# Performance work log

Measured on AMD Instinct MI355X. Metric: run time of the kernel, lower is better.

## Reference

```python
import jax, jax.numpy as jnp
import numpy as np

B, T, D, H = 512, 1024, 12, 100


def setup_inputs() -> dict:
    key = jax.random.key(0)
    ks = jax.random.split(key, 5)
    x = jax.random.normal(ks[0], (B, T, D), dtype=jnp.float32)
    Wx = jax.random.normal(ks[1], (D, 4 * H), dtype=jnp.float32) * (1.0 / np.sqrt(D))
    Wh = jax.random.normal(ks[2], (H, 4 * H), dtype=jnp.float32) * (1.0 / np.sqrt(H))
    b = jnp.zeros((4 * H,), dtype=jnp.float32)
    Wd = jax.random.normal(ks[3], (H, D), dtype=jnp.float32) * (1.0 / np.sqrt(H))
    bd = jnp.zeros((D,), dtype=jnp.float32)
    return {"x": x, "Wx": Wx, "Wh": Wh, "b": b, "Wd": Wd, "bd": bd}


def _lstm_seq(x, Wx, Wh, b):
    # Precompute input projection for all timesteps (vectorized GEMM).
    xg = jnp.einsum('btd,dh->bth', x, Wx) + b  # [B, T, 4H]
    xg = jnp.transpose(xg, (1, 0, 2))          # [T, B, 4H] for scan

    def step(carry, xg_t):
        h, c = carry
        z = xg_t + h @ Wh                      # [B, 4H]
        i, f, g, o = jnp.split(z, 4, axis=-1)  # Keras gate order: i, f, c, o
        i = jax.nn.sigmoid(i)
        f = jax.nn.sigmoid(f)
        g = jnp.tanh(g)
        o = jax.nn.sigmoid(o)
        c = f * c + i * g
        h = o * jnp.tanh(c)
        return (h, c), h

    h0 = jnp.zeros((x.shape[0], Wh.shape[0]), dtype=x.dtype)
    c0 = jnp.zeros_like(h0)
    _, hs = jax.lax.scan(step, (h0, c0), xg)   # hs: [T, B, H]
    return jnp.transpose(hs, (1, 0, 2))        # [B, T, H]


def reference(x, Wx, Wh, b, Wd, bd):
    hs = _lstm_seq(x, Wx, Wh, b)               # [B, T, H]
    return jnp.einsum('bth,hd->btd', hs, Wd) + bd  # [B, T, 12]
```

## Files before the change

kernel.cpp:

```cpp
#include <hip/hip_runtime.h>
#include <math.h>

#define T_LEN 1024
#define BATCH 512
#define DIN   12
#define HID   100
#define G4    400
#define MB    4
#define NBLK  (BATCH / MB)
#define AROW  160
#define NW    8
#define NTHR  (NW * 64)
#define CHUNK 64
#define UNROLL 8

typedef _Float16 half8   __attribute__((ext_vector_type(8)));
typedef _Float16 half4_t __attribute__((ext_vector_type(4)));
typedef float    f32x4   __attribute__((ext_vector_type(4)));

static __device__ __forceinline__ float fast_exp2(float v) {
#if __has_builtin(__builtin_amdgcn_exp2f)
    return __builtin_amdgcn_exp2f(v);
#else
    return exp2f(v);
#endif
}
static __device__ __forceinline__ float fast_rcp(float v) {
#if __has_builtin(__builtin_amdgcn_rcpf)
    return __builtin_amdgcn_rcpf(v);
#else
    return 1.0f / v;
#endif
}

__launch_bounds__(NTHR, 2)
__global__ void lstm_mfma_kernel(const float* __restrict__ x,
                                 const float* __restrict__ Wx,
                                 const float* __restrict__ Wh,
                                 const float* __restrict__ b,
                                 const float* __restrict__ Wd,
                                 const float* __restrict__ bd,
                                 float* __restrict__ out) {
    __shared__ __align__(16) char smem[65536];
    const int tid  = threadIdx.x;
    const int wid  = tid >> 6;
    const int lane = tid & 63;
    const int l    = lane & 15;
    const int quad = lane >> 4;
    const int b0   = blockIdx.x * MB;
    const int j    = wid * 16 + l;

    _Float16* stage = (_Float16*)smem;
    half8 bfrag[4][4];
#pragma unroll
    for (int pass = 0; pass < 2; ++pass) {
#pragma unroll
        for (int gg = 0; gg < 2; ++gg) {
            const int G = pass * 2 + gg;
#pragma unroll
            for (int kt = 0; kt < 4; ++kt) {
                half8 v;
#pragma unroll
                for (int jj = 0; jj < 8; ++jj) {
                    const int k = kt * 32 + quad * 8 + jj;
                    float w = 0.f;
                    if (wid < 7) {
                        if (j < HID) {
                            if (k < HID)            w = Wh[k * G4 + G * HID + j];
                            else if (k < HID + DIN) w = Wx[(k - HID) * G4 + G * HID + j];
                        }
                    } else if (G == 0) {
                        if (l < DIN && k < HID)     w = Wd[k * DIN + l];
                    }
                    v[jj] = (_Float16)w;
                }
                *(half8*)&stage[((wid * 8) + (gg * 4 + kt)) * 512 + lane * 8] = v;
            }
        }
        __syncthreads();
#pragma unroll
        for (int gg = 0; gg < 2; ++gg)
#pragma unroll
            for (int kt = 0; kt < 4; ++kt)
                bfrag[pass * 2 + gg][kt] =
                    *(half8*)&stage[((wid * 8) + (gg * 4 + kt)) * 512 + lane * 8];
        __syncthreads();
    }

    f32x4 biasC[4];
#pragma unroll
    for (int G = 0; G < 4; ++G) biasC[G] = (f32x4){0.f, 0.f, 0.f, 0.f};
    if (wid < 7) {
        if (j < HID) {
#pragma unroll
            for (int G = 0; G < 4; ++G) {
                const float bv = b[G * HID + j];
                biasC[G] = (f32x4){bv, bv, bv, bv};
            }
        }
    } else if (l < DIN) {
        const float bv = bd[l];
        biasC[0] = (f32x4){bv, bv, bv, bv};
    }

    _Float16 (*Ah)[MB][AROW] = (_Float16 (*)[MB][AROW])smem;
    _Float16* xchunk = (_Float16*)(smem + 2560);

    auto refill = [&](int c) {
#pragma unroll
        for (int ii = 0; ii < 2; ++ii) {
            const int f = tid + NTHR * ii;
            if (f < (CHUNK * MB * DIN) / 4) {
                const int m  = f / (CHUNK * DIN / 4);
                const int o  = f - m * (CHUNK * DIN / 4);
                const int tt = o / 3;
                const int dd = o - tt * 3;
                const float4 v = *(const float4*)(x +
                    ((size_t)(b0 + m) * T_LEN + c * CHUNK + tt) * DIN + dd * 4);
                half4_t h4;
                h4[0] = (_Float16)v.x; h4[1] = (_Float16)v.y;
                h4[2] = (_Float16)v.z; h4[3] = (_Float16)v.w;
                *(half4_t*)&xchunk[tt * (MB * DIN) + m * DIN + dd * 4] = h4;
            }
        }
    };

    for (int i = tid; i < (2 * MB * AROW) / 2; i += NTHR) ((int*)smem)[i] = 0;
    refill(0);
    __syncthreads();
    if (tid < MB * 3) {
        const int m = tid / 3, part = tid - (tid / 3) * 3;
        *(half4_t*)&Ah[0][m][HID + part * 4] =
            *(const half4_t*)&xchunk[m * DIN + part * 4];
    }
    __syncthreads();

    const bool gate_lane = (wid < 7) && (j < HID);
    const int  arow = l >> 2;
    const float L2E = 1.4426950408889634f;

    float c = 0.f;
    float obuf[UNROLL];

#pragma unroll 1
    for (int tb = 0; tb < T_LEN / UNROLL; ++tb) {
#pragma unroll
        for (int it = 0; it < UNROLL; ++it) {
            const int t  = tb * UNROLL + it;
            const int p  = it & 1;
            const int pn = p ^ 1;

            if (it == UNROLL - 1) {
                if (((tb + 1) & 7) == 0 && (tb + 1) < T_LEN / UNROLL) {
                    refill((tb + 1) >> 3);
                    __syncthreads();
                }
            }

            half8 a[4];
#pragma unroll
            for (int kt = 0; kt < 4; ++kt)
                a[kt] = *(const half8*)&Ah[p][arow][kt * 32 + quad * 8];

            if (wid < 7) {
                f32x4 acc[4];
#pragma unroll
                for (int kt = 0; kt < 4; ++kt)
#pragma unroll
                    for (int G = 0; G < 4; ++G)
                        acc[G] = __builtin_amdgcn_mfma_f32_16x16x32_f16(
                                     a[kt], bfrag[G][kt],
                                     (kt == 0) ? biasC[G] : acc[G], 0, 0, 0);

                if (gate_lane) {
                    const float ei = fast_exp2(-L2E * acc[0][0]);
                    const float ef = fast_exp2(-L2E * acc[1][0]);
                    const float eg = fast_exp2(-2.f * L2E * acc[2][0]);
                    const float eo = fast_exp2(-L2E * acc[3][0]);
                    const float gig = (1.f - eg) * fast_rcp((1.f + ei) * (1.f + eg));
                    const float gf  = fast_rcp(1.f + ef);
                    const float cn  = gf * c + gig;
                    c = cn;
                    const float ec = fast_exp2(-2.f * L2E * cn);
                    const float hv = (1.f - ec) * fast_rcp((1.f + eo) * (1.f + ec));
                    Ah[pn][quad][j] = (_Float16)hv;
                }
            } else {
                f32x4 accP;
#pragma unroll
                for (int kt = 0; kt < 4; ++kt)
                    accP = __builtin_amdgcn_mfma_f32_16x16x32_f16(
                               a[kt], bfrag[0][kt],
                               (kt == 0) ? biasC[0] : accP, 0, 0, 0);
                obuf[it] = accP[0];
                if ((t + 1) < T_LEN && lane < MB * 3) {
                    const int m = lane / 3, part = lane - (lane / 3) * 3;
                    *(half4_t*)&Ah[pn][m][HID + part * 4] =
                        *(const half4_t*)&xchunk[((t + 1) & (CHUNK - 1)) * (MB * DIN)
                                                 + m * DIN + part * 4];
                }
            }
            __syncthreads();
        }
        if (wid == 7 && l < DIN) {
#pragma unroll
            for (int s = 0; s < UNROLL; ++s) {
                const int row = tb * UNROLL + s - 1;
                if (row >= 0)
                    out[((size_t)(b0 + quad) * T_LEN + row) * DIN + l] = obuf[s];
            }
        }
    }

    if (wid == 7) {
        half8 a[4];
#pragma unroll
        for (int kt = 0; kt < 4; ++kt)
            a[kt] = *(const half8*)&Ah[0][arow][kt * 32 + quad * 8];
        f32x4 accP;
#pragma unroll
        for (int kt = 0; kt < 4; ++kt)
            accP = __builtin_amdgcn_mfma_f32_16x16x32_f16(
                       a[kt], bfrag[0][kt],
                       (kt == 0) ? biasC[0] : accP, 0, 0, 0);
        if (l < DIN)
            out[((size_t)(b0 + quad) * T_LEN + (T_LEN - 1)) * DIN + l] = accP[0];
    }
}

extern "C" void kernel_launch(void* const* d_in, const int* in_sizes, int n_in,
                              void* d_out, int out_size, void* d_ws, size_t ws_size,
                              hipStream_t stream) {
    const float* x  = (const float*)d_in[0];
    const float* Wx = (const float*)d_in[1];
    const float* Wh = (const float*)d_in[2];
    const float* b  = (const float*)d_in[3];
    const float* Wd = (const float*)d_in[4];
    const float* bd = (const float*)d_in[5];
    float* out = (float*)d_out;

    lstm_mfma_kernel<<<NBLK, NTHR, 0, stream>>>(x, Wx, Wh, b, Wd, bd, out);
}
```

Baseline: 536.4 us.

## Break MFMA accumulation chains, prescale gate weights, use lighter LDS barriers

Folds the -log2(e) (and -2log2(e) for the g gate) scaling into the weights and biases so the gate exponents need no multiply. The cell state is kept in the scaled domain. Each k-tile MFMA now writes an independent accumulator and the partial sums are added in scalar code, which removes the dependent MFMA chain on the serial recurrence path. __syncthreads is replaced by an lgkmcnt-only wait plus s_barrier. Output stores are also issued per step rather than buffered, trading more register pressure and a few extra adds for lower per-timestep latency.

```diff
diff --git a/kernel.cpp b/kernel.cpp
--- a/kernel.cpp
+++ b/kernel.cpp
@@ -31,6 +31,13 @@
 #else
     return 1.0f / v;
 #endif
+}
+
+static __device__ __forceinline__ void wg_barrier_lds() {
+    __builtin_amdgcn_sched_barrier(0);
+    asm volatile("s_waitcnt lgkmcnt(0)" ::: "memory");
+    __builtin_amdgcn_s_barrier();
+    __builtin_amdgcn_sched_barrier(0);
 }
 
 __launch_bounds__(NTHR, 2)
@@ -50,6 +57,8 @@
     const int b0   = blockIdx.x * MB;
     const int j    = wid * 16 + l;
 
+    const float L2E = 1.4426950408889634f;
+
     _Float16* stage = (_Float16*)smem;
     half8 bfrag[4][4];
 #pragma unroll
@@ -57,6 +66,7 @@
 #pragma unroll
         for (int gg = 0; gg < 2; ++gg) {
             const int G = pass * 2 + gg;
+            const float gsc = (G == 2) ? (-2.f * L2E) : (-L2E);
 #pragma unroll
             for (int kt = 0; kt < 4; ++kt) {
                 half8 v;
@@ -66,8 +76,8 @@
                     float w = 0.f;
                     if (wid < 7) {
                         if (j < HID) {
-                            if (k < HID)            w = Wh[k * G4 + G * HID + j];
-                            else if (k < HID + DIN) w = Wx[(k - HID) * G4 + G * HID + j];
+                            if (k < HID)            w = Wh[k * G4 + G * HID + j] * gsc;
+                            else if (k < HID + DIN) w = Wx[(k - HID) * G4 + G * HID + j] * gsc;
                         }
                     } else if (G == 0) {
                         if (l < DIN && k < HID)     w = Wd[k * DIN + l];
@@ -94,7 +104,8 @@
         if (j < HID) {
 #pragma unroll
             for (int G = 0; G < 4; ++G) {
-                const float bv = b[G * HID + j];
+                const float gsc = (G == 2) ? (-2.f * L2E) : (-L2E);
+                const float bv = b[G * HID + j] * gsc;
                 biasC[G] = (f32x4){bv, bv, bv, bv};
             }
         }
@@ -137,10 +148,9 @@
 
     const bool gate_lane = (wid < 7) && (j < HID);
     const int  arow = l >> 2;
-    const float L2E = 1.4426950408889634f;
-
-    float c = 0.f;
-    float obuf[UNROLL];
+    const f32x4 kZ = (f32x4){0.f, 0.f, 0.f, 0.f};
+
+    float cs = 0.f;
 
 #pragma unroll 1
     for (int tb = 0; tb < T_LEN / UNROLL; ++tb) {
@@ -153,7 +163,7 @@
             if (it == UNROLL - 1) {
                 if (((tb + 1) & 7) == 0 && (tb + 1) < T_LEN / UNROLL) {
                     refill((tb + 1) >> 3);
-                    __syncthreads();
+                    wg_barrier_lds();
                 }
             }
 
@@ -163,36 +173,41 @@
                 a[kt] = *(const half8*)&Ah[p][arow][kt * 32 + quad * 8];
 
             if (wid < 7) {
-                f32x4 acc[4];
+                f32x4 dg[4][4];
 #pragma unroll
                 for (int kt = 0; kt < 4; ++kt)
 #pragma unroll
                     for (int G = 0; G < 4; ++G)
-                        acc[G] = __builtin_amdgcn_mfma_f32_16x16x32_f16(
-                                     a[kt], bfrag[G][kt],
-                                     (kt == 0) ? biasC[G] : acc[G], 0, 0, 0);
+                        dg[G][kt] = __builtin_amdgcn_mfma_f32_16x16x32_f16(
+                                        a[kt], bfrag[G][kt],
+                                        (kt == 0) ? biasC[G] : kZ, 0, 0, 0);
 
                 if (gate_lane) {
-                    const float ei = fast_exp2(-L2E * acc[0][0]);
-                    const float ef = fast_exp2(-L2E * acc[1][0]);
-                    const float eg = fast_exp2(-2.f * L2E * acc[2][0]);
-                    const float eo = fast_exp2(-L2E * acc[3][0]);
-                    const float gig = (1.f - eg) * fast_rcp((1.f + ei) * (1.f + eg));
+                    const float zi = (dg[0][0][0] + dg[0][1][0]) + (dg[0][2][0] + dg[0][3][0]);
+                    const float zf = (dg[1][0][0] + dg[1][1][0]) + (dg[1][2][0] + dg[1][3][0]);
+                    const float zg = (dg[2][0][0] + dg[2][1][0]) + (dg[2][2][0] + dg[2][3][0]);
+                    const float zo = (dg[3][0][0] + dg[3][1][0]) + (dg[3][2][0] + dg[3][3][0]);
+                    const float ei = fast_exp2(zi);
+                    const float ef = fast_exp2(zf);
+                    const float eg = fast_exp2(zg);
+                    const float eo = fast_exp2(zo);
                     const float gf  = fast_rcp(1.f + ef);
-                    const float cn  = gf * c + gig;
-                    c = cn;
-                    const float ec = fast_exp2(-2.f * L2E * cn);
+                    const float dd  = (1.f + ei) * (1.f + eg);
+                    const float u   = __builtin_fmaf(eg, 2.f * L2E, -2.f * L2E);
+                    const float gig = u * fast_rcp(dd);
+                    cs = __builtin_fmaf(gf, cs, gig);
+                    const float ec = fast_exp2(cs);
                     const float hv = (1.f - ec) * fast_rcp((1.f + eo) * (1.f + ec));
                     Ah[pn][quad][j] = (_Float16)hv;
                 }
             } else {
-                f32x4 accP;
-#pragma unroll
-                for (int kt = 0; kt < 4; ++kt)
-                    accP = __builtin_amdgcn_mfma_f32_16x16x32_f16(
-                               a[kt], bfrag[0][kt],
-                               (kt == 0) ? biasC[0] : accP, 0, 0, 0);
-                obuf[it] = accP[0];
+                f32x4 p0 = __builtin_amdgcn_mfma_f32_16x16x32_f16(a[0], bfrag[0][0], biasC[0], 0, 0, 0);
+                f32x4 p1 = __builtin_amdgcn_mfma_f32_16x16x32_f16(a[1], bfrag[0][1], kZ, 0, 0, 0);
+                f32x4 p2 = __builtin_amdgcn_mfma_f32_16x16x32_f16(a[2], bfrag[0][2], kZ, 0, 0, 0);
+                f32x4 p3 = __builtin_amdgcn_mfma_f32_16x16x32_f16(a[3], bfrag[0][3], kZ, 0, 0, 0);
+                const float ov = (p0[0] + p1[0]) + (p2[0] + p3[0]);
+                if (t >= 1 && l < DIN)
+                    out[((size_t)(b0 + quad) * T_LEN + (t - 1)) * DIN + l] = ov;
                 if ((t + 1) < T_LEN && lane < MB * 3) {
                     const int m = lane / 3, part = lane - (lane / 3) * 3;
                     *(half4_t*)&Ah[pn][m][HID + part * 4] =
@@ -200,15 +215,7 @@
                                                  + m * DIN + part * 4];
                 }
             }
-            __syncthreads();
-        }
-        if (wid == 7 && l < DIN) {
-#pragma unroll
-            for (int s = 0; s < UNROLL; ++s) {
-                const int row = tb * UNROLL + s - 1;
-                if (row >= 0)
-                    out[((size_t)(b0 + quad) * T_LEN + row) * DIN + l] = obuf[s];
-            }
+            wg_barrier_lds();
         }
     }
 
@@ -217,14 +224,13 @@
 #pragma unroll
         for (int kt = 0; kt < 4; ++kt)
             a[kt] = *(const half8*)&Ah[0][arow][kt * 32 + quad * 8];
-        f32x4 accP;
-#pragma unroll
-        for (int kt = 0; kt < 4; ++kt)
-            accP = __builtin_amdgcn_mfma_f32_16x16x32_f16(
-                       a[kt], bfrag[0][kt],
-                       (kt == 0) ? biasC[0] : accP, 0, 0, 0);
+        f32x4 p0 = __builtin_amdgcn_mfma_f32_16x16x32_f16(a[0], bfrag[0][0], biasC[0], 0, 0, 0);
+        f32x4 p1 = __builtin_amdgcn_mfma_f32_16x16x32_f16(a[1], bfrag[0][1], kZ, 0, 0, 0);
+        f32x4 p2 = __builtin_amdgcn_mfma_f32_16x16x32_f16(a[2], bfrag[0][2], kZ, 0, 0, 0);
+        f32x4 p3 = __builtin_amdgcn_mfma_f32_16x16x32_f16(a[3], bfrag[0][3], kZ, 0, 0, 0);
+        const float ov = (p0[0] + p1[0]) + (p2[0] + p3[0]);
         if (l < DIN)
-            out[((size_t)(b0 + quad) * T_LEN + (T_LEN - 1)) * DIN + l] = accP[0];
+            out[((size_t)(b0 + quad) * T_LEN + (T_LEN - 1)) * DIN + l] = ov;
     }
 }
 
```

After: 579.1 us. 7.9% more time.
